# Optimization experiments

Hardware: AMD Instinct MI355X
Metric: run time of the kernel (lower is better)

## Reference

```python
import jax, jax.numpy as jnp
import numpy as np

BETA = 0.85
THR = 1.0
SLOPE = 25.0  # fast_sigmoid surrogate slope

@jax.custom_vjp
def spike_fn(v):
    # Heaviside fire with fast-sigmoid surrogate gradient (snntorch fast_sigmoid)
    return (v > 0).astype(v.dtype)

def _spike_fwd(v):
    return (v > 0).astype(v.dtype), v

def _spike_bwd(v, g):
    return (g / (SLOPE * jnp.abs(v) + 1.0) ** 2,)

spike_fn.defvjp(_spike_fwd, _spike_bwd)

def setup_inputs() -> dict:
    key = jax.random.key(0)
    k1, k2, k3, k4, k5 = jax.random.split(key, 5)
    B, T, IN, H = 32, 2048, 512, 256
    x = jax.random.normal(k1, (B, T, IN), dtype=jnp.float32)
    s_in = 1.0 / np.sqrt(IN)
    s_h = 1.0 / np.sqrt(H)
    W_in = jax.random.uniform(k2, (H, IN), jnp.float32, -s_in, s_in)
    b_in = jax.random.uniform(k3, (H,), jnp.float32, -s_in, s_in)
    V = jax.random.uniform(k4, (H, H), jnp.float32, -s_h, s_h)   # RLeaky recurrent linear
    b_rec = jax.random.uniform(k5, (H,), jnp.float32, -s_h, s_h)
    return {"x": x, "W_in": W_in, "b_in": b_in, "V": V, "b_rec": b_rec}

def reference(x, W_in, b_in, V, b_rec):
    B, T, _ = x.shape
    H = W_in.shape[0]
    # input projection for all timesteps at once: (B,T,H) -> (T,B,H)
    proj = jnp.einsum('bti,hi->bth', x, W_in) + b_in
    proj_t = jnp.transpose(proj, (1, 0, 2))

    def step(carry, p_t):
        spk, mem = carry
        input_ = p_t + spk                       # combined = proj[:,t] + spk
        rec = spk @ V.T + b_rec                   # RLeaky recurrent term
        reset = jax.lax.stop_gradient((mem > THR).astype(mem.dtype))
        mem = BETA * mem + input_ + rec - reset * THR  # subtract reset
        spk = spike_fn(mem - THR)
        return (spk, mem), spk

    init = (jnp.zeros((B, H), x.dtype), jnp.zeros((B, H), x.dtype))
    _, spikes = jax.lax.scan(step, init, proj_t)  # (T,B,H)
    return jnp.transpose(spikes, (1, 0, 2))       # (B,T,H)
```

## Files before the change

### kernel.cpp

```cpp
#include <hip/hip_runtime.h>
#include <cstddef>
#include <cstdint>

#define kB 32
#define kT 2048
#define kIn 512
#define kH 256
#define kBeta 0.85f
#define kThr 1.0f

#define N_SCAN kB
#define N_GEMM (kB * 8)
#define FLAGS_PER_B 8
#define TBURST 8

#define GBM 256
#define GBK 16
#define GLDA 260
#define SMEM_FLOATS (2 * GBK * GLDA)

#define SSTRIDE 260

__device__ __forceinline__ void wait_flag(int* f) {
    while (__hip_atomic_load(f, __ATOMIC_ACQUIRE, __HIP_MEMORY_SCOPE_AGENT) == 0) {
        __builtin_amdgcn_s_sleep(2);
    }
}

__device__ void gemm_body(const float* __restrict__ A,
                          const float* __restrict__ W,
                          const float* __restrict__ bias,
                          float* __restrict__ P,
                          int* flags, int gid, float* smem)
{
    float* As = smem;
    float* Bs = smem + GBK * GLDA;
    const int tid = threadIdx.x;
    const int b  = gid & 31;
    const int tt = gid >> 5;
    const int bm = b * kT + tt * GBM;
    const int tx = tid & 31;
    const int ty = tid >> 5;

    float acc[8][8];
#pragma unroll
    for (int i = 0; i < 8; ++i)
#pragma unroll
        for (int j = 0; j < 8; ++j) acc[i][j] = 0.f;

    const int r = tid >> 2, kc = (tid & 3) << 2;

    for (int kb = 0; kb < kIn; kb += GBK) {
        const float4 av = *reinterpret_cast<const float4*>(A + (size_t)(bm + r) * kIn + kb + kc);
        const float4 bv = *reinterpret_cast<const float4*>(W + (size_t)r * kIn + kb + kc);
        __syncthreads();
        As[(kc + 0) * GLDA + r] = av.x;
        As[(kc + 1) * GLDA + r] = av.y;
        As[(kc + 2) * GLDA + r] = av.z;
        As[(kc + 3) * GLDA + r] = av.w;
        Bs[(kc + 0) * GLDA + r] = bv.x;
        Bs[(kc + 1) * GLDA + r] = bv.y;
        Bs[(kc + 2) * GLDA + r] = bv.z;
        Bs[(kc + 3) * GLDA + r] = bv.w;
        __syncthreads();

#pragma unroll
        for (int k = 0; k < GBK; ++k) {
            const float4 aa0 = *reinterpret_cast<const float4*>(&As[k * GLDA + ty * 4]);
            const float4 aa1 = *reinterpret_cast<const float4*>(&As[k * GLDA + ty * 4 + 128]);
            const float4 bb0 = *reinterpret_cast<const float4*>(&Bs[k * GLDA + tx * 4]);
            const float4 bb1 = *reinterpret_cast<const float4*>(&Bs[k * GLDA + tx * 4 + 128]);
            const float av8[8] = {aa0.x, aa0.y, aa0.z, aa0.w, aa1.x, aa1.y, aa1.z, aa1.w};
            const float bv8[8] = {bb0.x, bb0.y, bb0.z, bb0.w, bb1.x, bb1.y, bb1.z, bb1.w};
#pragma unroll
            for (int i = 0; i < 8; ++i)
#pragma unroll
                for (int j = 0; j < 8; ++j)
                    acc[i][j] = fmaf(av8[i], bv8[j], acc[i][j]);
        }
    }

    const float4 bl = *reinterpret_cast<const float4*>(bias + tx * 4);
    const float4 bh = *reinterpret_cast<const float4*>(bias + tx * 4 + 128);
#pragma unroll
    for (int i = 0; i < 8; ++i) {
        const int m = bm + ty * 4 + (i & 3) + ((i >> 2) << 7);
        float4 o0, o1;
        o0.x = acc[i][0] + bl.x; o0.y = acc[i][1] + bl.y;
        o0.z = acc[i][2] + bl.z; o0.w = acc[i][3] + bl.w;
        o1.x = acc[i][4] + bh.x; o1.y = acc[i][5] + bh.y;
        o1.z = acc[i][6] + bh.z; o1.w = acc[i][7] + bh.w;
        *reinterpret_cast<float4*>(P + (size_t)m * kH + tx * 4) = o0;
        *reinterpret_cast<float4*>(P + (size_t)m * kH + tx * 4 + 128) = o1;
    }

    __syncthreads();
    if (flags && tid == 0) {
        __threadfence();
        atomicAdd(flags + b * FLAGS_PER_B + tt, 1);
    }
}

__device__ void scan_body(float* __restrict__ PO,
                          const float* __restrict__ V,
                          const float* __restrict__ brec,
                          int* flags, float* smem)
{
    unsigned long long* smask = reinterpret_cast<unsigned long long*>(smem);
    float* pbuf = smem + 16;

    const int b = blockIdx.x;
    const int tid = threadIdx.x;
    const int w = tid >> 6;
    const int l = tid & 63;
    const int h0 = l << 2;
    const int kc = w << 4;
    const bool owner = (tid < kH);
    const int h = tid & (kH - 1);

    float Vr[4][16];
#pragma unroll
    for (int i = 0; i < 4; ++i) {
        const float4* vp = reinterpret_cast<const float4*>(V + (size_t)(h0 + i) * kH + kc);
#pragma unroll
        for (int c4 = 0; c4 < 4; ++c4) {
            const float4 v = vp[c4];
            Vr[i][c4 * 4 + 0] = v.x; Vr[i][c4 * 4 + 1] = v.y;
            Vr[i][c4 * 4 + 2] = v.z; Vr[i][c4 * 4 + 3] = v.w;
        }
    }

    const float br = owner ? brec[h] : 0.f;
    float mem = 0.f, spk = 0.f;
    float* base = PO + (size_t)b * (size_t)kT * kH + h;

    if (tid < 4) smask[tid] = 0ull;

    int* bflags = flags ? (flags + b * FLAGS_PER_B) : nullptr;

    float pb[TBURST], pb2[TBURST], sst[TBURST];
    if (owner) {
        if (bflags) wait_flag(bflags + 0);
#pragma unroll
        for (int i = 0; i < TBURST; ++i) pb[i] = base[(size_t)i * kH];
    }
    __syncthreads();

    const int mshift = (w & 3) << 4;

    for (int tb = 0; tb < kT / TBURST; ++tb) {
#pragma unroll
        for (int ti = 0; ti < TBURST; ++ti) {

            if (owner && ti == 0) {
                if (tb > 0) {
#pragma unroll
                    for (int i = 0; i < TBURST; ++i)
                        base[(size_t)((tb - 1) * TBURST + i) * kH] = sst[i];
                }
                const int nb = tb + 1;
                if (bflags && nb < (kT / TBURST) && (nb & 31) == 0)
                    wait_flag(bflags + (nb >> 5));
#pragma unroll
                for (int i = 0; i < TBURST; ++i) {
                    int tt2 = nb * TBURST + i;
                    if (tt2 > kT - 1) tt2 = kT - 1;
                    pb2[i] = base[(size_t)tt2 * kH];
                }
            }

            const unsigned long long m = smask[w >> 2];
            const uint32_t chunk =
                __builtin_amdgcn_readfirstlane((uint32_t)(m >> mshift)) & 0xFFFFu;

            float a0 = 0.f, a1 = 0.f, a2 = 0.f, a3 = 0.f;
#pragma unroll
            for (int n = 0; n < 4; ++n) {
                const uint32_t nib = (chunk >> (n * 4)) & 0xFu;
                if (nib) {
#pragma unroll
                    for (int bit = 0; bit < 4; ++bit) {
                        const int j = n * 4 + bit;
                        const float bf = (float)((nib >> bit) & 1u);
                        a0 = fmaf(bf, Vr[0][j], a0);
                        a1 = fmaf(bf, Vr[1][j], a1);
                        a2 = fmaf(bf, Vr[2][j], a2);
                        a3 = fmaf(bf, Vr[3][j], a3);
                    }
                }
            }
            float4 part; part.x = a0; part.y = a1; part.z = a2; part.w = a3;
            *reinterpret_cast<float4*>(pbuf + w * SSTRIDE + h0) = part;

            __syncthreads();

            if (owner) {
                float s0  = pbuf[ 0 * SSTRIDE + h], s1  = pbuf[ 1 * SSTRIDE + h];
                float s2  = pbuf[ 2 * SSTRIDE + h], s3  = pbuf[ 3 * SSTRIDE + h];
                float s4  = pbuf[ 4 * SSTRIDE + h], s5  = pbuf[ 5 * SSTRIDE + h];
                float s6  = pbuf[ 6 * SSTRIDE + h], s7  = pbuf[ 7 * SSTRIDE + h];
                float s8  = pbuf[ 8 * SSTRIDE + h], s9  = pbuf[ 9 * SSTRIDE + h];
                float s10 = pbuf[10 * SSTRIDE + h], s11 = pbuf[11 * SSTRIDE + h];
                float s12 = pbuf[12 * SSTRIDE + h], s13 = pbuf[13 * SSTRIDE + h];
                float s14 = pbuf[14 * SSTRIDE + h], s15 = pbuf[15 * SSTRIDE + h];
                const float r0 = (s0 + s1) + (s2 + s3);
                const float r1 = (s4 + s5) + (s6 + s7);
                const float r2 = (s8 + s9) + (s10 + s11);
                const float r3 = (s12 + s13) + (s14 + s15);
                const float rec = ((r0 + r1) + (r2 + r3)) + br;
                const float p = pb[ti];
                float m2;
                {
#pragma clang fp contract(off)
                    const float input_ = p + spk;
                    m2 = kBeta * mem;
                    m2 = m2 + input_;
                    m2 = m2 + rec;
                    m2 = m2 - spk * kThr;
                }
                const bool fire = (m2 > kThr);
                const float ns = fire ? 1.0f : 0.0f;
                const unsigned long long bm = __ballot(fire);
                if ((tid & 63) == 0) smask[tid >> 6] = bm;
                mem = m2;
                spk = ns;
                sst[ti] = ns;
            }

            __syncthreads();
        }
        if (owner) {
#pragma unroll
            for (int i = 0; i < TBURST; ++i) pb[i] = pb2[i];
        }
    }

    if (owner) {
#pragma unroll
        for (int i = 0; i < TBURST; ++i)
            base[(size_t)((kT / TBURST - 1) * TBURST + i) * kH] = sst[i];
    }
}

__global__ void __launch_bounds__(1024, 4)
fused(const float* __restrict__ x, const float* __restrict__ W,
      const float* __restrict__ b_in, const float* __restrict__ V,
      const float* __restrict__ b_rec, float* __restrict__ PO,
      int* flags, int n_scan)
{
    __shared__ __align__(16) float smem[SMEM_FLOATS];
    if ((int)blockIdx.x < n_scan) {
        scan_body(PO, V, b_rec, flags, smem);
    } else {
        gemm_body(x, W, b_in, PO, flags, (int)blockIdx.x - n_scan, smem);
    }
}

extern "C" void kernel_launch(void* const* d_in, const int* in_sizes, int n_in,
                              void* d_out, int out_size, void* d_ws, size_t ws_size,
                              hipStream_t stream) {
    const float* x     = (const float*)d_in[0];
    const float* W_in  = (const float*)d_in[1];
    const float* b_in  = (const float*)d_in[2];
    const float* V     = (const float*)d_in[3];
    const float* b_rec = (const float*)d_in[4];
    float* out = (float*)d_out;

    const size_t flag_bytes = (size_t)N_SCAN * FLAGS_PER_B * sizeof(int);
    if (ws_size >= flag_bytes) {
        int* flags = (int*)d_ws;
        hipMemsetAsync(flags, 0, flag_bytes, stream);
        fused<<<N_SCAN + N_GEMM, 1024, 0, stream>>>(x, W_in, b_in, V, b_rec,
                                                    out, flags, N_SCAN);
    } else {
        fused<<<N_GEMM, 1024, 0, stream>>>(x, W_in, b_in, V, b_rec, out, nullptr, 0);
        fused<<<N_SCAN, 1024, 0, stream>>>(x, W_in, b_in, V, b_rec, out, nullptr, N_SCAN);
    }
}
```

Measured before the change: 1.760 ms.

## Offload scan prefetch and spike writeback to dedicated waves via LDS ring

In the recurrent scan block, the owner threads no longer do their own per-thread global loads of the projection and stores of spikes. Wave 15 prefetches the next eight timesteps with float4 loads into a double-buffered LDS ring, and wave 14 writes the previous burst's spikes back from an LDS output buffer. __syncthreads is replaced with an lgkmcnt wait plus s_barrier. The aim is to take global memory latency and vmcnt waits off the serial critical path of the time loop, at the cost of more LDS traffic and extra coordination between waves.

```diff
diff --git a/kernel.cpp b/kernel.cpp
--- a/kernel.cpp
+++ b/kernel.cpp
@@ -12,19 +12,28 @@
 #define N_SCAN kB
 #define N_GEMM (kB * 8)
 #define FLAGS_PER_B 8
-#define TBURST 8
 
 #define GBM 256
 #define GBK 16
 #define GLDA 260
-#define SMEM_FLOATS (2 * GBK * GLDA)
 
 #define SSTRIDE 260
+#define SM_PBUF 16
+#define SM_PRING (SM_PBUF + 16 * SSTRIDE)
+#define SM_OBUF  (SM_PRING + 16 * 256)
+#define SMEM_SCAN (SM_OBUF + 8 * 256)
+#define SMEM_GEMM (2 * GBK * GLDA)
+#define SMEM_FLOATS (SMEM_SCAN > SMEM_GEMM ? SMEM_SCAN : SMEM_GEMM)
 
 __device__ __forceinline__ void wait_flag(int* f) {
     while (__hip_atomic_load(f, __ATOMIC_ACQUIRE, __HIP_MEMORY_SCOPE_AGENT) == 0) {
         __builtin_amdgcn_s_sleep(2);
     }
+}
+
+__device__ __forceinline__ void scan_bar() {
+    asm volatile("s_waitcnt lgkmcnt(0)" ::: "memory");
+    __builtin_amdgcn_s_barrier();
 }
 
 __device__ void gemm_body(const float* __restrict__ A,
@@ -107,7 +116,9 @@
                           int* flags, float* smem)
 {
     unsigned long long* smask = reinterpret_cast<unsigned long long*>(smem);
-    float* pbuf = smem + 16;
+    float* pbuf  = smem + SM_PBUF;
+    float* pring = smem + SM_PRING;
+    float* obuf  = smem + SM_OBUF;
 
     const int b = blockIdx.x;
     const int tid = threadIdx.x;
@@ -132,42 +143,66 @@
 
     const float br = owner ? brec[h] : 0.f;
     float mem = 0.f, spk = 0.f;
-    float* base = PO + (size_t)b * (size_t)kT * kH + h;
+    float* po_b = PO + (size_t)b * (size_t)kT * kH;
 
     if (tid < 4) smask[tid] = 0ull;
 
     int* bflags = flags ? (flags + b * FLAGS_PER_B) : nullptr;
 
-    float pb[TBURST], pb2[TBURST], sst[TBURST];
-    if (owner) {
+    if (w == 15) {
         if (bflags) wait_flag(bflags + 0);
 #pragma unroll
-        for (int i = 0; i < TBURST; ++i) pb[i] = base[(size_t)i * kH];
-    }
-    __syncthreads();
+        for (int r = 0; r < 8; ++r) {
+            const float4 v = *reinterpret_cast<const float4*>(po_b + (size_t)r * kH + 4 * l);
+            *reinterpret_cast<float4*>(pring + r * 256 + 4 * l) = v;
+        }
+    }
+    scan_bar();
 
     const int mshift = (w & 3) << 4;
 
-    for (int tb = 0; tb < kT / TBURST; ++tb) {
-#pragma unroll
-        for (int ti = 0; ti < TBURST; ++ti) {
-
-            if (owner && ti == 0) {
-                if (tb > 0) {
-#pragma unroll
-                    for (int i = 0; i < TBURST; ++i)
-                        base[(size_t)((tb - 1) * TBURST + i) * kH] = sst[i];
+    for (int tb = 0; tb < kT / 8; ++tb) {
+        float4 g0, g1, g2, g3, g4, g5, g6, g7;
+#pragma unroll
+        for (int ti = 0; ti < 8; ++ti) {
+            const int t = tb * 8 + ti;
+
+            if (ti == 0) {
+                if (w == 15 && tb < kT / 8 - 1) {
+                    if (bflags && ((tb + 1) & 31) == 0 && ((tb + 1) >> 5) < 8)
+                        wait_flag(bflags + ((tb + 1) >> 5));
+                    const size_t r0 = (size_t)(tb * 8 + 8) * kH + 4 * l;
+                    g0 = *reinterpret_cast<const float4*>(po_b + r0 + 0 * kH);
+                    g1 = *reinterpret_cast<const float4*>(po_b + r0 + 1 * kH);
+                    g2 = *reinterpret_cast<const float4*>(po_b + r0 + 2 * kH);
+                    g3 = *reinterpret_cast<const float4*>(po_b + r0 + 3 * kH);
+                    g4 = *reinterpret_cast<const float4*>(po_b + r0 + 4 * kH);
+                    g5 = *reinterpret_cast<const float4*>(po_b + r0 + 5 * kH);
+                    g6 = *reinterpret_cast<const float4*>(po_b + r0 + 6 * kH);
+                    g7 = *reinterpret_cast<const float4*>(po_b + r0 + 7 * kH);
                 }
-                const int nb = tb + 1;
-                if (bflags && nb < (kT / TBURST) && (nb & 31) == 0)
-                    wait_flag(bflags + (nb >> 5));
-#pragma unroll
-                for (int i = 0; i < TBURST; ++i) {
-                    int tt2 = nb * TBURST + i;
-                    if (tt2 > kT - 1) tt2 = kT - 1;
-                    pb2[i] = base[(size_t)tt2 * kH];
+                if (w == 14 && tb > 0) {
+#pragma unroll
+                    for (int r = 0; r < 8; ++r) {
+                        const float4 v = *reinterpret_cast<const float4*>(obuf + r * 256 + 4 * l);
+                        *reinterpret_cast<float4*>(po_b + (size_t)((tb - 1) * 8 + r) * kH + 4 * l) = v;
+                    }
                 }
             }
+            if (ti == 2 && w == 15 && tb < kT / 8 - 1) {
+                const int s0 = (tb & 1) ? 0 : 8;
+                *reinterpret_cast<float4*>(pring + (s0 + 0) * 256 + 4 * l) = g0;
+                *reinterpret_cast<float4*>(pring + (s0 + 1) * 256 + 4 * l) = g1;
+                *reinterpret_cast<float4*>(pring + (s0 + 2) * 256 + 4 * l) = g2;
+                *reinterpret_cast<float4*>(pring + (s0 + 3) * 256 + 4 * l) = g3;
+                *reinterpret_cast<float4*>(pring + (s0 + 4) * 256 + 4 * l) = g4;
+                *reinterpret_cast<float4*>(pring + (s0 + 5) * 256 + 4 * l) = g5;
+                *reinterpret_cast<float4*>(pring + (s0 + 6) * 256 + 4 * l) = g6;
+                *reinterpret_cast<float4*>(pring + (s0 + 7) * 256 + 4 * l) = g7;
+            }
+
+            float pld = 0.f;
+            if (owner) pld = pring[(t & 15) * 256 + h];
 
             const unsigned long long m = smask[w >> 2];
             const uint32_t chunk =
@@ -192,7 +227,7 @@
             float4 part; part.x = a0; part.y = a1; part.z = a2; part.w = a3;
             *reinterpret_cast<float4*>(pbuf + w * SSTRIDE + h0) = part;
 
-            __syncthreads();
+            scan_bar();
 
             if (owner) {
                 float s0  = pbuf[ 0 * SSTRIDE + h], s1  = pbuf[ 1 * SSTRIDE + h];
@@ -208,7 +243,7 @@
                 const float r2 = (s8 + s9) + (s10 + s11);
                 const float r3 = (s12 + s13) + (s14 + s15);
                 const float rec = ((r0 + r1) + (r2 + r3)) + br;
-                const float p = pb[ti];
+                const float p = pld;
                 float m2;
                 {
 #pragma clang fp contract(off)
@@ -222,23 +257,21 @@
                 const float ns = fire ? 1.0f : 0.0f;
                 const unsigned long long bm = __ballot(fire);
                 if ((tid & 63) == 0) smask[tid >> 6] = bm;
+                obuf[ti * 256 + h] = ns;
                 mem = m2;
                 spk = ns;
-                sst[ti] = ns;
             }
 
-            __syncthreads();
-        }
-        if (owner) {
-#pragma unroll
-            for (int i = 0; i < TBURST; ++i) pb[i] = pb2[i];
-        }
-    }
-
-    if (owner) {
-#pragma unroll
-        for (int i = 0; i < TBURST; ++i)
-            base[(size_t)((kT / TBURST - 1) * TBURST + i) * kH] = sst[i];
+            scan_bar();
+        }
+    }
+
+    if (w == 14) {
+#pragma unroll
+        for (int r = 0; r < 8; ++r) {
+            const float4 v = *reinterpret_cast<const float4*>(obuf + r * 256 + 4 * l);
+            *reinterpret_cast<float4*>(po_b + (size_t)((kT / 8 - 1) * 8 + r) * kH + 4 * l) = v;
+        }
     }
 }
 
```

New measurement: 1.804 ms. 1.03x slower.
